# Performance work log

Measured on AMD Instinct MI355X. Metric: run time of the kernel, lower is better.

## Reference

```python
import jax, jax.numpy as jnp
import numpy as np

DIM = 512; H = 8; DH = 64; M = 256; ITERS = 6; K = 33  # residual conv kernel


def _pinv(x, iters=ITERS):
    # Moore-Penrose iterative pseudo-inverse (lucidrains moore_penrose_iter_pinv)
    abs_x = jnp.abs(x)
    denom = abs_x.sum(-1).max() * abs_x.sum(-2).max()  # global max of col/row sums
    z = jnp.swapaxes(x, -1, -2) / denom
    I = jnp.eye(x.shape[-1], dtype=x.dtype)
    for _ in range(iters):
        xz = x @ z
        z = 0.25 * z @ (13. * I - xz @ (15. * I - xz @ (7. * I - xz)))
    return z


def setup_inputs() -> dict:
    key = jax.random.key(0)
    ks = jax.random.split(key, 5)
    b, n = 4, 4096
    inner = H * DH
    x = jax.random.normal(ks[0], (b, n, DIM), jnp.float32)
    ln_g = jnp.ones((DIM,), jnp.float32)
    ln_b = jnp.zeros((DIM,), jnp.float32)
    w_qkv = jax.random.normal(ks[1], (DIM, 3 * inner), jnp.float32) / np.sqrt(DIM).astype(np.float32)
    w_out = jax.random.normal(ks[2], (inner, DIM), jnp.float32) / np.sqrt(inner).astype(np.float32)
    b_out = jnp.zeros((DIM,), jnp.float32)
    res_w = jax.random.normal(ks[3], (H, K), jnp.float32) * 0.02  # depthwise conv weight per head
    return {"x": x, "ln_g": ln_g, "ln_b": ln_b, "w_qkv": w_qkv,
            "w_out": w_out, "b_out": b_out, "res_w": res_w}


def reference(x, ln_g, ln_b, w_qkv, w_out, b_out, res_w):
    b, n, d = x.shape
    # LayerNorm (eps=1e-5, biased variance, like torch)
    mu = x.mean(-1, keepdims=True)
    var = ((x - mu) ** 2).mean(-1, keepdims=True)
    xn = (x - mu) * jax.lax.rsqrt(var + 1e-5) * ln_g + ln_b
    # QKV projection, no bias
    qkv = xn @ w_qkv  # [b, n, 3*h*dh]
    q, k, v = jnp.split(qkv, 3, axis=-1)
    tohd = lambda t: t.reshape(b, n, H, DH).transpose(0, 2, 1, 3)  # b h n d
    q = tohd(q) * (DH ** -0.5)
    k = tohd(k)
    v = tohd(v)
    # landmarks: mean over consecutive blocks of l = n // M (n divisible by M here)
    l = n // M
    q_l = q.reshape(b, H, M, l, DH).mean(3)  # b h m d
    k_l = k.reshape(b, H, M, l, DH).mean(3)
    attn1 = jax.nn.softmax(jnp.einsum('bhid,bhjd->bhij', q, k_l), axis=-1)   # b h n m
    attn2 = jax.nn.softmax(jnp.einsum('bhid,bhjd->bhij', q_l, k_l), axis=-1)  # b h m m
    attn3 = jax.nn.softmax(jnp.einsum('bhid,bhjd->bhij', q_l, k), axis=-1)   # b h m n
    out = (attn1 @ _pinv(attn2)) @ (attn3 @ v)  # b h n dh
    # depthwise residual conv over sequence dim (Conv2d(heads, heads, (33,1), groups=heads))
    res = jax.lax.conv_general_dilated(
        v, res_w.reshape(H, 1, K, 1), (1, 1), ((K // 2, K // 2), (0, 0)),
        feature_group_count=H, dimension_numbers=('NCHW', 'OIHW', 'NCHW'))
    out = out + res
    # merge heads + output projection (dropout is identity at eval)
    out = out.transpose(0, 2, 1, 3).reshape(b, n, H * DH) @ w_out + b_out
    # TransLayer residual
    return x + out
```

## Files before the change

kernel.cpp:

```cpp
#include <hip/hip_runtime.h>
#include <hip/hip_bf16.h>

#define SEQ    4096
#define NBAT   4
#define NHEAD  8
#define NBH    32
#define DMODEL 512
#define DHEAD  64
#define NLM    256
#define NSP    4

typedef __attribute__((ext_vector_type(8))) short s8v;
typedef __attribute__((ext_vector_type(4))) float f4v;

__device__ __forceinline__ float b2f(unsigned short u){
  union { unsigned int i; float f; } v; v.i = ((unsigned int)u) << 16; return v.f;
}
__device__ __forceinline__ unsigned short f2b(float f){
  union { float f; unsigned int i; } v; v.f = f;
  unsigned int r = v.i + 0x7fffu + ((v.i >> 16) & 1u);
  return (unsigned short)(r >> 16);
}
__device__ __forceinline__ s8v ldg8(const unsigned short* p){
  return *reinterpret_cast<const s8v*>(p);
}
__device__ __forceinline__ f4v mfma16(s8v a, s8v b, f4v c){
  return __builtin_amdgcn_mfma_f32_16x16x32_bf16(a, b, c, 0, 0, 0);
}
__device__ __forceinline__ f4v zero4(){ f4v z; z[0]=0.f; z[1]=0.f; z[2]=0.f; z[3]=0.f; return z; }
__device__ __forceinline__ void gload16(const unsigned short* g, unsigned short* l){
  __builtin_amdgcn_global_load_lds((const __attribute__((address_space(1))) unsigned int*)g,
                                   (__attribute__((address_space(3))) unsigned int*)l, 16, 0, 0);
}

__global__ void k_prep(const float* __restrict__ wqkv, const float* __restrict__ wout,
                       unsigned short* __restrict__ wqkvT, unsigned short* __restrict__ woutT,
                       unsigned int* __restrict__ denomU){
  int t = blockIdx.x*256 + threadIdx.x;
  if (t == 0) denomU[0] = 0u;
  if (t < 786432){ int kk = t/1536, n = t%1536; wqkvT[(size_t)n*512 + kk] = f2b(wqkv[t]); }
  else { int t2 = t - 786432; if (t2 < 262144){ int kk = t2/512, n = t2%512; woutT[(size_t)n*512 + kk] = f2b(wout[t2]); } }
}

__global__ __launch_bounds__(256) void k_ln(const float* __restrict__ x, const float* __restrict__ g,
                                            const float* __restrict__ be, unsigned short* __restrict__ xn){
  int row = blockIdx.x*4 + (threadIdx.x>>6);
  int l = threadIdx.x & 63;
  const float* xr = x + (size_t)row*DMODEL;
  float4 a = *(const float4*)(xr + l*4);
  float4 b = *(const float4*)(xr + 256 + l*4);
  float s = a.x+a.y+a.z+a.w + b.x+b.y+b.z+b.w;
  float q = a.x*a.x+a.y*a.y+a.z*a.z+a.w*a.w + b.x*b.x+b.y*b.y+b.z*b.z+b.w*b.w;
  #pragma unroll
  for (int m=1;m<64;m<<=1){ s += __shfl_xor(s,m); q += __shfl_xor(q,m); }
  float mean = s*(1.f/DMODEL);
  float rstd = rsqrtf(q*(1.f/DMODEL) - mean*mean + 1e-5f);
  int c0 = l*4, c1 = 256 + l*4;
  float av[4] = {a.x,a.y,a.z,a.w}, bv[4] = {b.x,b.y,b.z,b.w};
  ushort4 u0, u1;
  unsigned short* p0 = (unsigned short*)&u0; unsigned short* p1 = (unsigned short*)&u1;
  #pragma unroll
  for (int e=0;e<4;++e){
    p0[e] = f2b((av[e]-mean)*rstd*g[c0+e] + be[c0+e]);
    p1[e] = f2b((bv[e]-mean)*rstd*g[c1+e] + be[c1+e]);
  }
  *(ushort4*)(xn + (size_t)row*DMODEL + c0) = u0;
  *(ushort4*)(xn + (size_t)row*DMODEL + c1) = u1;
}

__device__ __forceinline__ void gemm512v2(const unsigned short* __restrict__ A, const unsigned short* __restrict__ B,
                                          int m0, int n0, int t, unsigned short* lA, unsigned short* lB,
                                          f4v acc[4][4]){
  int w = t>>6, l = t&63;
  int wm = (w&1)*64, wn = (w>>1)*64;
  int g = l>>4, qi = l&15;
  int rs = (w<<4) + (l>>2);
  int s0 = l&3;
  int c0 = ((s0 ^ ((rs>>1)&3)) << 3);
  int r1 = rs + 64;
  int c1 = ((s0 ^ ((r1>>1)&3)) << 3);
  const unsigned short* gA0 = A + (size_t)(m0+rs)*DMODEL + c0;
  const unsigned short* gA1 = A + (size_t)(m0+r1)*DMODEL + c1;
  const unsigned short* gB0 = B + (size_t)(n0+rs)*DMODEL + c0;
  const unsigned short* gB1 = B + (size_t)(n0+r1)*DMODEL + c1;
  unsigned short* dA0 = lA + (w<<9);
  unsigned short* dA1 = lA + 2048 + (w<<9);
  unsigned short* dB0 = lB + (w<<9);
  unsigned short* dB1 = lB + 2048 + (w<<9);
  int aofs[4], bofs[4];
  #pragma unroll
  for (int i=0;i<4;++i){
    int ra = wm + i*16 + qi;
    aofs[i] = ra*32 + ((g ^ ((ra>>1)&3))<<3);
    int rb = wn + i*16 + qi;
    bofs[i] = rb*32 + ((g ^ ((rb>>1)&3))<<3);
  }
  for (int ks=0; ks<16; ++ks){
    gload16(gA0, dA0); gload16(gA1, dA1);
    gload16(gB0, dB0); gload16(gB1, dB1);
    gA0 += 32; gA1 += 32; gB0 += 32; gB1 += 32;
    __syncthreads();
    s8v af[4], bf[4];
    #pragma unroll
    for (int i=0;i<4;++i) af[i] = *(s8v*)&lA[aofs[i]];
    #pragma unroll
    for (int j=0;j<4;++j) bf[j] = *(s8v*)&lB[bofs[j]];
    #pragma unroll
    for (int i=0;i<4;++i)
      #pragma unroll
      for (int j=0;j<4;++j) acc[i][j] = mfma16(af[i], bf[j], acc[i][j]);
    __syncthreads();
  }
}

__global__ __launch_bounds__(256) void k_gqkv(const unsigned short* __restrict__ xn, const unsigned short* __restrict__ wT,
                                              unsigned short* __restrict__ q, unsigned short* __restrict__ k,
                                              unsigned short* __restrict__ v, unsigned short* __restrict__ vT){
  __shared__ __align__(16) unsigned short lA[4096], lB[4096];
  int b0 = blockIdx.x;
  int bid = (b0 & 7) * 192 + (b0 >> 3);
  int mblk = bid/12, nblk = bid%12;
  int m0 = mblk*128, n0 = nblk*128;
  int t = threadIdx.x;
  f4v acc[4][4];
  #pragma unroll
  for (int i=0;i<4;++i)
    #pragma unroll
    for (int j=0;j<4;++j) acc[i][j] = zero4();
  gemm512v2(xn, wT, m0, n0, t, lA, lB, acc);
  int w = t>>6, l = t&63; int wm = (w&1)*64, wn = (w>>1)*64;
  int part = nblk >> 2;
  int coff = (nblk & 3) * 128;
  unsigned short* dst = (part==0) ? q : (part==1) ? k : v;
  float scale = (part==0) ? 0.125f : 1.f;
  #pragma unroll
  for (int i=0;i<4;++i)
  #pragma unroll
  for (int j=0;j<4;++j){
    int colg = coff + wn + j*16 + (l&15);
    int h = colg>>6, c = colg&63;
    #pragma unroll
    for (int r=0;r<4;++r){
      int rowg = m0 + wm + i*16 + ((l>>4)<<2) + r;
      int b = rowg>>12, n = rowg&4095;
      unsigned short val = f2b(acc[i][j][r]*scale);
      dst[ (((size_t)(b*NHEAD + h))*SEQ + n)*DHEAD + c ] = val;
      if (part == 2)
        vT[ (((size_t)(b*NHEAD + h))*DHEAD + c)*SEQ + n ] = val;
    }
  }
}

__global__ __launch_bounds__(256) void k_gout(const unsigned short* __restrict__ ao, const unsigned short* __restrict__ wT,
                                              const float* __restrict__ x, const float* __restrict__ bo,
                                              float* __restrict__ out){
  __shared__ __align__(16) unsigned short lA[4096], lB[4096];
  int b0 = blockIdx.x;
  int bid = (b0 & 7) * 64 + (b0 >> 3);
  int mblk = bid>>2, nblk = bid&3;
  int m0 = mblk*128, n0 = nblk*128;
  int t = threadIdx.x;
  f4v acc[4][4];
  #pragma unroll
  for (int i=0;i<4;++i)
    #pragma unroll
    for (int j=0;j<4;++j) acc[i][j] = zero4();
  gemm512v2(ao, wT, m0, n0, t, lA, lB, acc);
  int w = t>>6, l = t&63; int wm = (w&1)*64, wn = (w>>1)*64;
  #pragma unroll
  for (int i=0;i<4;++i)
  #pragma unroll
  for (int j=0;j<4;++j){
    int colg = n0 + wn + j*16 + (l&15);
    #pragma unroll
    for (int r=0;r<4;++r){
      int rowg = m0 + wm + i*16 + ((l>>4)<<2) + r;
      size_t ad = (size_t)rowg*DMODEL + colg;
      out[ad] = acc[i][j][r] + x[ad] + bo[colg];
    }
  }
}

__global__ void k_lmk(const unsigned short* __restrict__ q, const unsigned short* __restrict__ k,
                      unsigned short* __restrict__ ql, unsigned short* __restrict__ kl){
  int tg = blockIdx.x*256 + threadIdx.x;
  int c4 = (tg&15)*4, m = (tg>>4)&255, bh = tg>>12;
  const unsigned short* qb = q + ((size_t)bh*SEQ + m*16)*DHEAD + c4;
  const unsigned short* kb = k + ((size_t)bh*SEQ + m*16)*DHEAD + c4;
  float s0=0.f,s1=0.f,s2=0.f,s3=0.f, t0=0.f,t1=0.f,t2=0.f,t3=0.f;
  #pragma unroll
  for (int j=0;j<16;++j){
    ushort4 uq = *(const ushort4*)(qb + (size_t)j*DHEAD);
    ushort4 uk = *(const ushort4*)(kb + (size_t)j*DHEAD);
    s0+=b2f(uq.x); s1+=b2f(uq.y); s2+=b2f(uq.z); s3+=b2f(uq.w);
    t0+=b2f(uk.x); t1+=b2f(uk.y); t2+=b2f(uk.z); t3+=b2f(uk.w);
  }
  ushort4 oq, ok;
  oq.x=f2b(s0*(1.f/16.f)); oq.y=f2b(s1*(1.f/16.f)); oq.z=f2b(s2*(1.f/16.f)); oq.w=f2b(s3*(1.f/16.f));
  ok.x=f2b(t0*(1.f/16.f)); ok.y=f2b(t1*(1.f/16.f)); ok.z=f2b(t2*(1.f/16.f)); ok.w=f2b(t3*(1.f/16.f));
  *(ushort4*)(ql + ((size_t)bh*NLM + m)*DHEAD + c4) = oq;
  *(ushort4*)(kl + ((size_t)bh*NLM + m)*DHEAD + c4) = ok;
}

__global__ __launch_bounds__(512) void k_attn2(const unsigned short* __restrict__ ql, const unsigned short* __restrict__ kl,
                                               unsigned short* __restrict__ a2, unsigned short* __restrict__ a2t,
                                               unsigned int* __restrict__ denomU){
  __shared__ float cs[256];
  int bh = blockIdx.x; int t = threadIdx.x; int w = t>>6, l = t&63;
  const unsigned short* Q = ql + (size_t)bh*NLM*DHEAD;
  const unsigned short* K = kl + (size_t)bh*NLM*DHEAD;
  f4v acc[2][16];
  #pragma unroll
  for (int i=0;i<2;++i)
    #pragma unroll
    for (int j=0;j<16;++j) acc[i][j] = zero4();
  int m0 = w*32;
  #pragma unroll
  for (int ks=0; ks<2; ++ks){
    int kk = ks*32 + ((l>>4)<<3);
    s8v af0 = ldg8(&Q[(size_t)(m0 + (l&15))*DHEAD + kk]);
    s8v af1 = ldg8(&Q[(size_t)(m0 + 16 + (l&15))*DHEAD + kk]);
    #pragma unroll
    for (int j=0;j<16;++j){
      s8v bf = ldg8(&K[(size_t)(j*16 + (l&15))*DHEAD + kk]);
      acc[0][j] = mfma16(af0, bf, acc[0][j]);
      acc[1][j] = mfma16(af1, bf, acc[1][j]);
    }
  }
  #pragma unroll
  for (int i=0;i<2;++i)
  #pragma unroll
  for (int r=0;r<4;++r){
    float mx = -1e30f;
    #pragma unroll
    for (int j=0;j<16;++j) mx = fmaxf(mx, acc[i][j][r]);
    #pragma unroll
    for (int mm=1;mm<16;mm<<=1) mx = fmaxf(mx, __shfl_xor(mx,mm));
    float sm = 0.f;
    #pragma unroll
    for (int j=0;j<16;++j){ float p = __expf(acc[i][j][r]-mx); acc[i][j][r]=p; sm += p; }
    #pragma unroll
    for (int mm=1;mm<16;mm<<=1) sm += __shfl_xor(sm,mm);
    float inv = 1.f/sm;
    #pragma unroll
    for (int j=0;j<16;++j) acc[i][j][r] *= inv;
  }
  for (int e=t; e<256; e+=512) cs[e] = 0.f;
  __syncthreads();
  size_t b0 = (size_t)bh*NLM*NLM;
  #pragma unroll
  for (int i=0;i<2;++i)
  #pragma unroll
  for (int j=0;j<16;++j){
    int col = j*16 + (l&15);
    int rowb = m0 + i*16 + ((l>>4)<<2);
    float csp = 0.f;
    #pragma unroll
    for (int r=0;r<4;++r){
      float p = acc[i][j][r];
      unsigned short pb = f2b(p);
      a2 [b0 + (size_t)(rowb+r)*NLM + col] = pb;
      a2t[b0 + (size_t)col*NLM + rowb + r] = pb;
      csp += p;
    }
    csp += __shfl_xor(csp, 16); csp += __shfl_xor(csp, 32);
    if ((l>>4) == 0) atomicAdd(&cs[col], csp);
  }
  __syncthreads();
  if (t < 256) atomicMax(denomU, __float_as_uint(cs[t]));
}

__global__ __launch_bounds__(256) void k_a3w2p(const unsigned short* __restrict__ ql, const unsigned short* __restrict__ kb,
                                               const unsigned short* __restrict__ vT,
                                               float* __restrict__ po, float* __restrict__ pm, float* __restrict__ pd){
  __shared__ __align__(16) unsigned short Ks[256*64];
  __shared__ __align__(16) unsigned short Vs[64*256];
  int bid = blockIdx.x;
  int ksp = bid & 3;
  int qp  = (bid >> 2) & 3;
  int bh  = bid >> 4;
  int t = threadIdx.x, w = t>>6, l = t&63;
  int q0 = qp*64 + w*16;
  int g = l>>4, qi = l&15;
  const unsigned short* Q = ql + ((size_t)bh*NLM + q0)*DHEAD;
  const unsigned short* K = kb + (size_t)bh*SEQ*DHEAD;
  const unsigned short* V = vT + (size_t)bh*DHEAD*SEQ;
  s8v bq0 = ldg8(&Q[(size_t)qi*DHEAD + g*8]);
  s8v bq1 = ldg8(&Q[(size_t)qi*DHEAD + 32 + g*8]);
  float m_run = -1e30f, den = 0.f;
  f4v oacc[4];
  #pragma unroll
  for (int j=0;j<4;++j) oacc[j] = zero4();
  int sl0 = ((g&1)*2)*16 + qi;
  int jsel = g>>1;
  for (int kc = ksp*4; kc < ksp*4+4; ++kc){
    const unsigned short* Kc = K + (size_t)kc*256*DHEAD;
    #pragma unroll
    for (int it2=0; it2<8; ++it2){
      int cid = it2*256 + t;
      int row = cid>>3, cl = cid&7;
      gload16(&Kc[(size_t)(row<<6) + ((cl^(row&7))<<3)], Ks + it2*2048 + w*512);
      int row2 = cid>>5, cl2 = cid&31;
      gload16(&V[(size_t)row2*SEQ + kc*256 + ((cl2^(row2&7))<<3)], Vs + it2*2048 + 16384 - 16384 + w*512 + 0);
    }
    __syncthreads();
    f4v acc[16];
    #pragma unroll
    for (int j=0;j<16;++j) acc[j] = zero4();
    #pragma unroll
    for (int ks=0;ks<2;++ks){
      s8v bq = (ks==0) ? bq0 : bq1;
      #pragma unroll
      for (int j=0;j<16;++j){
        int r = j*16+qi;
        s8v ak = *(s8v*)&Ks[(size_t)(r<<6) + (((ks*4+g) ^ (qi&7))<<3)];
        acc[j] = mfma16(ak, bq, acc[j]);
      }
    }
    float cm = -1e30f;
    #pragma unroll
    for (int j=0;j<16;++j)
      cm = fmaxf(cm, fmaxf(fmaxf(acc[j][0],acc[j][1]), fmaxf(acc[j][2],acc[j][3])));
    cm = fmaxf(cm, __shfl_xor(cm,16));
    cm = fmaxf(cm, __shfl_xor(cm,32));
    float nm = fmaxf(m_run, cm);
    float f = __expf(m_run - nm);
    m_run = nm;
    float ls = 0.f;
    unsigned int pku[32];
    #pragma unroll
    for (int j=0;j<16;++j){
      float p0 = __expf(acc[j][0]-nm), p1 = __expf(acc[j][1]-nm);
      float p2 = __expf(acc[j][2]-nm), p3 = __expf(acc[j][3]-nm);
      ls += (p0+p1)+(p2+p3);
      pku[2*j+0] = (unsigned int)f2b(p0) | ((unsigned int)f2b(p1)<<16);
      pku[2*j+1] = (unsigned int)f2b(p2) | ((unsigned int)f2b(p3)<<16);
    }
    den = den*f + ls;
    float fr0 = __shfl(f, g*4+0, 64), fr1 = __shfl(f, g*4+1, 64);
    float fr2 = __shfl(f, g*4+2, 64), fr3 = __shfl(f, g*4+3, 64);
    #pragma unroll
    for (int j=0;j<4;++j){
      oacc[j][0]*=fr0; oacc[j][1]*=fr1; oacc[j][2]*=fr2; oacc[j][3]*=fr3;
    }
    #pragma unroll
    for (int ks=0;ks<8;++ks){
      unsigned int w0a = (unsigned int)__shfl((int)pku[4*ks+0], sl0, 64);
      unsigned int w1a = (unsigned int)__shfl((int)pku[4*ks+1], sl0, 64);
      unsigned int w0b = (unsigned int)__shfl((int)pku[4*ks+2], sl0, 64);
      unsigned int w1b = (unsigned int)__shfl((int)pku[4*ks+3], sl0, 64);
      unsigned int w2a = (unsigned int)__shfl((int)pku[4*ks+0], sl0+16, 64);
      unsigned int w3a = (unsigned int)__shfl((int)pku[4*ks+1], sl0+16, 64);
      unsigned int w2b = (unsigned int)__shfl((int)pku[4*ks+2], sl0+16, 64);
      unsigned int w3b = (unsigned int)__shfl((int)pku[4*ks+3], sl0+16, 64);
      unsigned int wv0 = jsel ? w0b : w0a;
      unsigned int wv1 = jsel ? w1b : w1a;
      unsigned int wv2 = jsel ? w2b : w2a;
      unsigned int wv3 = jsel ? w3b : w3a;
      s8v af;
      af[0] = (short)(wv0&0xffff); af[1] = (short)(wv0>>16);
      af[2] = (short)(wv1&0xffff); af[3] = (short)(wv1>>16);
      af[4] = (short)(wv2&0xffff); af[5] = (short)(wv2>>16);
      af[6] = (short)(wv3&0xffff); af[7] = (short)(wv3>>16);
      int ch = ks*4 + g;
      #pragma unroll
      for (int j=0;j<4;++j){
        int r = j*16+qi;
        s8v bu = *(s8v*)&Vs[(size_t)(r<<8) + ((ch ^ (qi&7))<<3)];
        oacc[j] = mfma16(af, bu, oacc[j]);
      }
    }
    __syncthreads();
  }
  den += __shfl_xor(den,16); den += __shfl_xor(den,32);
  #pragma unroll
  for (int j=0;j<4;++j)
    #pragma unroll
    for (int r=0;r<4;++r)
      po[(((size_t)(ksp*NBH + bh))*NLM + q0 + g*4 + r)*DHEAD + j*16 + qi] = oacc[j][r];
  if (g == 0){
    pm[(size_t)(ksp*NBH + bh)*NLM + q0 + qi] = m_run;
    pd[(size_t)(ksp*NBH + bh)*NLM + q0 + qi] = den;
  }
}

__global__ __launch_bounds__(256) void k_a3c(const float* __restrict__ po, const float* __restrict__ pm,
                                             const float* __restrict__ pd, unsigned short* __restrict__ w2t){
  int tg = blockIdx.x*256 + threadIdx.x;
  int bh = tg >> 12; int c = (tg >> 6) & 63; int r4 = (tg & 63) << 2;
  ushort4 ov;
  unsigned short* op = (unsigned short*)&ov;
  #pragma unroll
  for (int rr=0; rr<4; ++rr){
    int row = r4 + rr;
    float m[NSP];
    float gm = -1e30f;
    #pragma unroll
    for (int s=0;s<NSP;++s){ m[s] = pm[(size_t)(s*NBH+bh)*NLM + row]; gm = fmaxf(gm, m[s]); }
    float den = 0.f, o = 0.f;
    #pragma unroll
    for (int s=0;s<NSP;++s){
      float wsc = __expf(m[s]-gm);
      den += pd[(size_t)(s*NBH+bh)*NLM + row]*wsc;
      o   += po[(((size_t)(s*NBH+bh))*NLM + row)*DHEAD + c]*wsc;
    }
    op[rr] = f2b(o/den);
  }
  *(ushort4*)&w2t[(size_t)bh*DHEAD*NLM + (size_t)c*NLM + r4] = ov;
}

__global__ __launch_bounds__(256) void k_conv(const unsigned short* __restrict__ v, const float* __restrict__ rw,
                                              unsigned short* __restrict__ cf){
  int bh = blockIdx.x >> 6;
  int n0 = (blockIdx.x & 63) * 64;
  int h = bh & 7, b = bh >> 3;
  int t = threadIdx.x;
  int tx = t & 15, ty = t >> 4;
  int c4 = tx * 4;
  int nb = n0 + ty * 4;
  const unsigned short* vb = v + ((size_t)bh * SEQ) * DHEAD + c4;
  ushort4 val[36];
  #pragma unroll
  for (int i = 0; i < 36; ++i){
    int nn = nb - 16 + i;
    if (nn >= 0 && nn < SEQ) val[i] = *(const ushort4*)(vb + (size_t)nn * DHEAD);
    else { val[i].x = 0; val[i].y = 0; val[i].z = 0; val[i].w = 0; }
  }
  float wgt[33];
  #pragma unroll
  for (int o = 0; o < 33; ++o) wgt[o] = rw[h*33 + o];
  #pragma unroll
  for (int i = 0; i < 4; ++i){
    float s0 = 0.f, s1 = 0.f, s2 = 0.f, s3 = 0.f;
    #pragma unroll
    for (int o = 0; o < 33; ++o){
      ushort4 u = val[i + o];
      float w0 = wgt[o];
      s0 += w0 * b2f(u.x); s1 += w0 * b2f(u.y);
      s2 += w0 * b2f(u.z); s3 += w0 * b2f(u.w);
    }
    ushort4 ov;
    ov.x = f2b(s0); ov.y = f2b(s1); ov.z = f2b(s2); ov.w = f2b(s3);
    size_t ad = ((size_t)b * SEQ + (nb + i)) * DMODEL + h * DHEAD + c4;
    *(ushort4*)(cf + ad) = ov;
  }
}

__device__ __forceinline__ void pcore(const unsigned short* __restrict__ Ab, const unsigned short* __restrict__ Bb,
                                      int m0, int n0, int l, f4v acc[4][4]){
  for (int ks=0; ks<8; ++ks){
    int kk = ks*32 + ((l>>4)<<3);
    s8v af[4], bf[4];
    #pragma unroll
    for (int i=0;i<4;++i) af[i] = ldg8(&Ab[(size_t)(m0 + i*16 + (l&15))*256 + kk]);
    #pragma unroll
    for (int j=0;j<4;++j) bf[j] = ldg8(&Bb[(size_t)(n0 + j*16 + (l&15))*256 + kk]);
    #pragma unroll
    for (int i=0;i<4;++i)
      #pragma unroll
      for (int j=0;j<4;++j) acc[i][j] = mfma16(af[i], bf[j], acc[i][j]);
  }
}


__global__ __launch_bounds__(64) void k_x0(const unsigned short* __restrict__ a2,
                                           unsigned short* __restrict__ XN, unsigned short* __restrict__ XT,
                                           const unsigned int* __restrict__ denomU){
  int bid = blockIdx.x;
  int bh = bid>>4, tt = bid&15;
  int m0 = (tt>>2)*64, n0 = (tt&3)*64;
  int l = threadIdx.x;
  size_t bb = (size_t)bh*65536;
  f4v acc[4][4];
  #pragma unroll
  for (int i=0;i<4;++i)
    #pragma unroll
    for (int j=0;j<4;++j) acc[i][j] = zero4();
  pcore(a2+bb, a2+bb, m0, n0, l, acc);
  float s = 1.f/__uint_as_float(denomU[0]);
  #pragma unroll
  for (int i=0;i<4;++i)
  #pragma unroll
  for (int j=0;j<4;++j){
    int col = n0 + j*16 + (l&15);
    #pragma unroll
    for (int r=0;r<4;++r){
      int row = m0 + i*16 + ((l>>4)<<2) + r;
      unsigned short ob = f2b(acc[i][j][r]*s);
      XN[bb + (size_t)row*256 + col] = ob;
      XT[bb + (size_t)col*256 + row] = ob;
    }
  }
}

__global__ __launch_bounds__(64) void k_l1(const unsigned short* __restrict__ XN, const unsigned short* __restrict__ XT,
                                           const unsigned short* __restrict__ zsrc,
                                           unsigned short* __restrict__ YN, unsigned short* __restrict__ YT,
                                           unsigned short* __restrict__ CT,
                                           unsigned short* __restrict__ WN, unsigned short* __restrict__ EN){
  int bid = blockIdx.x;
  int part = bid>>9; bid &= 511;
  int bh = bid>>4, tt = bid&15;
  int m0 = (tt>>2)*64, n0 = (tt&3)*64;
  int l = threadIdx.x;
  size_t bb = (size_t)bh*65536;
  f4v acc[4][4];
  #pragma unroll
  for (int i=0;i<4;++i)
    #pragma unroll
    for (int j=0;j<4;++j) acc[i][j] = zero4();
  if (part == 0){
    pcore(XN+bb, XT+bb, m0, n0, l, acc);
    #pragma unroll
    for (int i=0;i<4;++i)
    #pragma unroll
    for (int j=0;j<4;++j){
      int col = n0 + j*16 + (l&15);
      #pragma unroll
      for (int r=0;r<4;++r){
        int row = m0 + i*16 + ((l>>4)<<2) + r;
        float y = acc[i][j][r];
        float xv = b2f(XN[bb + (size_t)row*256 + col]);
        unsigned short yb = f2b(y);
        YN[bb + (size_t)row*256 + col] = yb;
        YT[bb + (size_t)col*256 + row] = yb;
        CT[bb + (size_t)col*256 + row] = f2b(7.f*xv - y);
      }
    }
  } else {
    pcore(zsrc+bb, XT+bb, m0, n0, l, acc);
    #pragma unroll
    for (int i=0;i<4;++i)
    #pragma unroll
    for (int j=0;j<4;++j){
      int col = n0 + j*16 + (l&15);
      #pragma unroll
      for (int r=0;r<4;++r){
        int row = m0 + i*16 + ((l>>4)<<2) + r;
        size_t idx = bb + (size_t)row*256 + col;
        float wv = acc[i][j][r];
        float zv = b2f(zsrc[idx]);
        WN[idx] = f2b(wv);
        EN[idx] = f2b(7.f*zv - wv);
      }
    }
  }
}

__global__ __launch_bounds__(64) void k_l2(unsigned short* __restrict__ XN, unsigned short* __restrict__ XT,
                                           const unsigned short* __restrict__ zsrc, unsigned short* __restrict__ zdst,
                                           const unsigned short* __restrict__ YN, const unsigned short* __restrict__ YT,
                                           const unsigned short* __restrict__ CT,
                                           const unsigned short* __restrict__ WN, const unsigned short* __restrict__ EN,
                                           int zonly){
  int bid = blockIdx.x;
  int part;
  if (zonly){ part = 1; } else { part = bid>>9; bid &= 511; }
  int bh = bid>>4, tt = bid&15;
  int m0 = (tt>>2)*64, n0 = (tt&3)*64;
  int l = threadIdx.x;
  size_t bb = (size_t)bh*65536;
  f4v acc[4][4];
  #pragma unroll
  for (int i=0;i<4;++i)
    #pragma unroll
    for (int j=0;j<4;++j) acc[i][j] = zero4();
  if (part == 0){
    pcore(YN+bb, CT+bb, m0, n0, l, acc);
    #pragma unroll
    for (int i=0;i<4;++i)
    #pragma unroll
    for (int j=0;j<4;++j){
      int col = n0 + j*16 + (l&15);
      #pragma unroll
      for (int r=0;r<4;++r){
        int row = m0 + i*16 + ((l>>4)<<2) + r;
        size_t idx = bb + (size_t)row*256 + col;
        float xv = b2f(XN[idx]);
        float yv = b2f(YN[idx]);
        unsigned short ob = f2b(0.25f*(13.f*xv - 15.f*yv + acc[i][j][r]));
        XN[idx] = ob;
        XT[bb + (size_t)col*256 + row] = ob;
      }
    }
  } else {
    pcore(EN+bb, YT+bb, m0, n0, l, acc);
    #pragma unroll
    for (int i=0;i<4;++i)
    #pragma unroll
    for (int j=0;j<4;++j){
      int col = n0 + j*16 + (l&15);
      #pragma unroll
      for (int r=0;r<4;++r){
        int row = m0 + i*16 + ((l>>4)<<2) + r;
        size_t idx = bb + (size_t)row*256 + col;
        float zv = b2f(zsrc[idx]);
        float wv = b2f(WN[idx]);
        zdst[idx] = f2b(0.25f*(13.f*zv - 15.f*wv + acc[i][j][r]));
      }
    }
  }
}

__global__ __launch_bounds__(64) void k_ue(const unsigned short* __restrict__ z6, const unsigned short* __restrict__ w2t,
                                           unsigned short* __restrict__ ut, const unsigned int* __restrict__ denomU){
  int bid = blockIdx.x;
  int bh = bid>>2, tt = bid&3;
  int m0 = tt*64;
  int l = threadIdx.x;
  float dinv = 1.f/__uint_as_float(denomU[0]);
  f4v acc[4][4];
  #pragma unroll
  for (int i=0;i<4;++i)
    #pragma unroll
    for (int j=0;j<4;++j) acc[i][j] = zero4();
  pcore(z6 + (size_t)bh*65536, w2t + (size_t)bh*16384, m0, 0, l, acc);
  #pragma unroll
  for (int i=0;i<4;++i)
  #pragma unroll
  for (int j=0;j<4;++j){
    int col = j*16 + (l&15);
    #pragma unroll
    for (int r=0;r<4;++r){
      int row = m0 + i*16 + ((l>>4)<<2) + r;
      ut[(size_t)bh*16384 + (size_t)col*256 + row] = f2b(acc[i][j][r]*dinv);
    }
  }
}

__global__ __launch_bounds__(256) void k_attn1(const unsigned short* __restrict__ qb, const unsigned short* __restrict__ kl,
                                               const unsigned short* __restrict__ ut, const unsigned short* __restrict__ cf,
                                               unsigned short* __restrict__ ao){
  int bh = blockIdx.x>>6;
  int t = threadIdx.x, w = t>>6, l = t&63;
  int q0 = ((blockIdx.x&63)<<6) + (w<<4);
  int g = l>>4, qi = l&15;
  const unsigned short* Q = qb + (size_t)bh*SEQ*DHEAD;
  const unsigned short* K = kl + (size_t)bh*NLM*DHEAD;
  f4v acc[16];
  #pragma unroll
  for (int j=0;j<16;++j) acc[j] = zero4();
  #pragma unroll
  for (int ks=0;ks<2;++ks){
    int kk = ks*32 + g*8;
    s8v bq = ldg8(&Q[(size_t)(q0+qi)*DHEAD + kk]);
    #pragma unroll
    for (int j=0;j<16;++j){
      s8v ak = ldg8(&K[(size_t)(j*16+qi)*DHEAD + kk]);
      acc[j] = mfma16(ak, bq, acc[j]);
    }
  }
  float mx = -1e30f;
  #pragma unroll
  for (int j=0;j<16;++j)
    mx = fmaxf(mx, fmaxf(fmaxf(acc[j][0],acc[j][1]), fmaxf(acc[j][2],acc[j][3])));
  mx = fmaxf(mx, __shfl_xor(mx,16));
  mx = fmaxf(mx, __shfl_xor(mx,32));
  float sm = 0.f;
  #pragma unroll
  for (int j=0;j<16;++j)
    #pragma unroll
    for (int r=0;r<4;++r){ float p = __expf(acc[j][r]-mx); acc[j][r]=p; sm += p; }
  sm += __shfl_xor(sm,16); sm += __shfl_xor(sm,32);
  float inv = 1.f/sm;
  unsigned int pku[32];
  #pragma unroll
  for (int j=0;j<16;++j){
    pku[2*j+0] = (unsigned int)f2b(acc[j][0]*inv) | ((unsigned int)f2b(acc[j][1]*inv)<<16);
    pku[2*j+1] = (unsigned int)f2b(acc[j][2]*inv) | ((unsigned int)f2b(acc[j][3]*inv)<<16);
  }
  const unsigned short* U = ut + (size_t)bh*DHEAD*NLM;
  f4v oacc[4];
  #pragma unroll
  for (int j=0;j<4;++j) oacc[j] = zero4();
  int sl0 = ((g&1)*2)*16 + qi;
  int jsel = g>>1;
  #pragma unroll
  for (int ks=0;ks<8;++ks){
    unsigned int w0a = (unsigned int)__shfl((int)pku[4*ks+0], sl0, 64);
    unsigned int w1a = (unsigned int)__shfl((int)pku[4*ks+1], sl0, 64);
    unsigned int w0b = (unsigned int)__shfl((int)pku[4*ks+2], sl0, 64);
    unsigned int w1b = (unsigned int)__shfl((int)pku[4*ks+3], sl0, 64);
    unsigned int w2a = (unsigned int)__shfl((int)pku[4*ks+0], sl0+16, 64);
    unsigned int w3a = (unsigned int)__shfl((int)pku[4*ks+1], sl0+16, 64);
    unsigned int w2b = (unsigned int)__shfl((int)pku[4*ks+2], sl0+16, 64);
    unsigned int w3b = (unsigned int)__shfl((int)pku[4*ks+3], sl0+16, 64);
    unsigned int wv0 = jsel ? w0b : w0a;
    unsigned int wv1 = jsel ? w1b : w1a;
    unsigned int wv2 = jsel ? w2b : w2a;
    unsigned int wv3 = jsel ? w3b : w3a;
    s8v af;
    af[0] = (short)(wv0&0xffff); af[1] = (short)(wv0>>16);
    af[2] = (short)(wv1&0xffff); af[3] = (short)(wv1>>16);
    af[4] = (short)(wv2&0xffff); af[5] = (short)(wv2>>16);
    af[6] = (short)(wv3&0xffff); af[7] = (short)(wv3>>16);
    int mk = ks*32 + g*8;
    #pragma unroll
    for (int j=0;j<4;++j){
      s8v bu = ldg8(&U[(size_t)(j*16+qi)*NLM + mk]);
      oacc[j] = mfma16(af, bu, oacc[j]);
    }
  }
  int b = bh>>3, h = bh&7;
  #pragma unroll
  for (int j=0;j<4;++j){
    int c = j*16 + qi;
    #pragma unroll
    for (int r=0;r<4;++r){
      int n = q0 + g*4 + r;
      size_t ad = ((size_t)(b*SEQ + n))*DMODEL + h*DHEAD + c;
      ao[ad] = f2b(oacc[j][r] + b2f(cf[ad]));
    }
  }
}

extern "C" void kernel_launch(void* const* d_in, const int* in_sizes, int n_in,
                              void* d_out, int out_size, void* d_ws, size_t ws_size,
                              hipStream_t stream){
  const float* x    = (const float*)d_in[0];
  const float* lng  = (const float*)d_in[1];
  const float* lnb  = (const float*)d_in[2];
  const float* wqkv = (const float*)d_in[3];
  const float* wout = (const float*)d_in[4];
  const float* bout = (const float*)d_in[5];
  const float* resw = (const float*)d_in[6];
  float* out = (float*)d_out;

  char* ws = (char*)d_ws;
  size_t off = 0;
  auto alloc = [&](size_t bytes)->char*{ char* p = ws + off; off += (bytes + 255) & ~(size_t)255; return p; };

  unsigned short* wqkvT = (unsigned short*)alloc((size_t)1536*512*2);
  unsigned short* woutT = (unsigned short*)alloc((size_t)512*512*2);
  unsigned int*   denomU= (unsigned int*)  alloc(256);
  unsigned short* xn    = (unsigned short*)alloc((size_t)16384*512*2);
  unsigned short* XN = xn;
  unsigned short* XT = xn + (size_t)1*NBH*NLM*NLM;
  unsigned short* YN = xn + (size_t)2*NBH*NLM*NLM;
  unsigned short* YT = xn + (size_t)3*NBH*NLM*NLM;
  unsigned short* q   = (unsigned short*)alloc((size_t)NBH*SEQ*DHEAD*2);
  unsigned short* kb  = (unsigned short*)alloc((size_t)NBH*SEQ*DHEAD*2);
  unsigned short* ao  = kb;
  unsigned short* v   = (unsigned short*)alloc((size_t)NBH*SEQ*DHEAD*2);
  unsigned short* vT  = (unsigned short*)alloc((size_t)NBH*DHEAD*SEQ*2);
  unsigned short* ql  = (unsigned short*)alloc((size_t)NBH*NLM*DHEAD*2);
  unsigned short* kl  = (unsigned short*)alloc((size_t)NBH*NLM*DHEAD*2);
  unsigned short* a2  = (unsigned short*)alloc((size_t)NBH*NLM*NLM*2);
  unsigned short* a2t = (unsigned short*)alloc((size_t)NBH*NLM*NLM*2);
  unsigned short* convf = (unsigned short*)alloc((size_t)NBAT*SEQ*DMODEL*2);
  unsigned short* CTb = (unsigned short*)alloc((size_t)NBH*NLM*NLM*2);
  unsigned short* WN  = (unsigned short*)alloc((size_t)NBH*NLM*NLM*2);
  unsigned short* EN  = (unsigned short*)alloc((size_t)NBH*NLM*NLM*2);
  unsigned short* zP  = (unsigned short*)alloc((size_t)NBH*NLM*NLM*2);
  unsigned short* zQ  = (unsigned short*)alloc((size_t)NBH*NLM*NLM*2);
  float* po = (float*)alloc((size_t)NSP*NBH*NLM*DHEAD*4);
  float* pm = (float*)alloc((size_t)NSP*NBH*NLM*4);
  float* pd = (float*)alloc((size_t)NSP*NBH*NLM*4);
  unsigned short* w2t = (unsigned short*)alloc((size_t)NBH*DHEAD*NLM*2);
  unsigned short* ut  = (unsigned short*)alloc((size_t)NBH*DHEAD*NLM*2);
  (void)ws_size; (void)in_sizes; (void)n_in; (void)out_size;

  k_prep<<<4096,256,0,stream>>>(wqkv, wout, wqkvT, woutT, denomU);
  k_ln  <<<4096,256,0,stream>>>(x, lng, lnb, xn);
  k_gqkv<<<1536,256,0,stream>>>(xn, wqkvT, q, kb, v, vT);
  k_lmk <<<512,256,0,stream>>>(q, kb, ql, kl);
  k_attn2<<<32,512,0,stream>>>(ql, kl, a2, a2t, denomU);
  k_a3w2p<<<512,256,0,stream>>>(ql, kb, vT, po, pm, pd);
  k_a3c <<<512,256,0,stream>>>(po, pm, pd, w2t);
  k_conv<<<2048,256,0,stream>>>(v, resw, convf);

  k_x0<<<512,64,0,stream>>>(a2, XN, XT, denomU);
  unsigned short* zbuf[2] = {zP, zQ};
  const unsigned short* zs = a2t;
  for (int it = 0; it < 6; ++it){
    int zonly = (it==5) ? 1 : 0;
    k_l1<<<1024,64,0,stream>>>(XN, XT, zs, YN, YT, CTb, WN, EN);
    k_l2<<<zonly?512:1024,64,0,stream>>>(XN, XT, zs, zbuf[it&1], YN, YT, CTb, WN, EN, zonly);
    zs = zbuf[it&1];
  }
  k_ue<<<128,64,0,stream>>>(zs, w2t, ut, denomU);

  k_attn1<<<2048,256,0,stream>>>(q, kl, ut, convf, ao);
  k_gout <<<512,256,0,stream>>>(ao, woutT, x, bout, out);
}
```

Before: 566.5 us.

## Merge prep/LN and conv/landmark kernels; drop transposed copies in pinv iterations

Fuses the weight-conversion and LayerNorm kernels into one launch, and likewise the depthwise conv and landmark-mean kernels, to cut launch overhead and let independent work share the GPU. The pinv iteration no longer writes transposed copies (XT, YT, CT) and instead passes the same row-major buffer as the B operand to pcore, relying on symmetry or on pcore's operand convention to remove scattered transposed stores. The transposed-store removal is only correct if the matrices involved are symmetric or pcore reads B in the matching orientation, so it carries a correctness risk.

Measured after the change: 516.4 us. 1.1x faster.

```diff
diff --git a/kernel.cpp b/kernel.cpp
--- a/kernel.cpp
+++ b/kernel.cpp
@@ -33,39 +33,41 @@
                                    (__attribute__((address_space(3))) unsigned int*)l, 16, 0, 0);
 }
 
-__global__ void k_prep(const float* __restrict__ wqkv, const float* __restrict__ wout,
-                       unsigned short* __restrict__ wqkvT, unsigned short* __restrict__ woutT,
-                       unsigned int* __restrict__ denomU){
-  int t = blockIdx.x*256 + threadIdx.x;
-  if (t == 0) denomU[0] = 0u;
-  if (t < 786432){ int kk = t/1536, n = t%1536; wqkvT[(size_t)n*512 + kk] = f2b(wqkv[t]); }
-  else { int t2 = t - 786432; if (t2 < 262144){ int kk = t2/512, n = t2%512; woutT[(size_t)n*512 + kk] = f2b(wout[t2]); } }
-}
-
-__global__ __launch_bounds__(256) void k_ln(const float* __restrict__ x, const float* __restrict__ g,
-                                            const float* __restrict__ be, unsigned short* __restrict__ xn){
-  int row = blockIdx.x*4 + (threadIdx.x>>6);
-  int l = threadIdx.x & 63;
-  const float* xr = x + (size_t)row*DMODEL;
-  float4 a = *(const float4*)(xr + l*4);
-  float4 b = *(const float4*)(xr + 256 + l*4);
-  float s = a.x+a.y+a.z+a.w + b.x+b.y+b.z+b.w;
-  float q = a.x*a.x+a.y*a.y+a.z*a.z+a.w*a.w + b.x*b.x+b.y*b.y+b.z*b.z+b.w*b.w;
-  #pragma unroll
-  for (int m=1;m<64;m<<=1){ s += __shfl_xor(s,m); q += __shfl_xor(q,m); }
-  float mean = s*(1.f/DMODEL);
-  float rstd = rsqrtf(q*(1.f/DMODEL) - mean*mean + 1e-5f);
-  int c0 = l*4, c1 = 256 + l*4;
-  float av[4] = {a.x,a.y,a.z,a.w}, bv[4] = {b.x,b.y,b.z,b.w};
-  ushort4 u0, u1;
-  unsigned short* p0 = (unsigned short*)&u0; unsigned short* p1 = (unsigned short*)&u1;
-  #pragma unroll
-  for (int e=0;e<4;++e){
-    p0[e] = f2b((av[e]-mean)*rstd*g[c0+e] + be[c0+e]);
-    p1[e] = f2b((bv[e]-mean)*rstd*g[c1+e] + be[c1+e]);
-  }
-  *(ushort4*)(xn + (size_t)row*DMODEL + c0) = u0;
-  *(ushort4*)(xn + (size_t)row*DMODEL + c1) = u1;
+__global__ __launch_bounds__(256) void k_prepln(const float* __restrict__ wqkv, const float* __restrict__ wout,
+                                                const float* __restrict__ x, const float* __restrict__ g,
+                                                const float* __restrict__ be,
+                                                unsigned short* __restrict__ wqkvT, unsigned short* __restrict__ woutT,
+                                                unsigned short* __restrict__ xn, unsigned int* __restrict__ denomU){
+  int b0 = blockIdx.x;
+  if (b0 < 4096){
+    int t = b0*256 + threadIdx.x;
+    if (t == 0) denomU[0] = 0u;
+    if (t < 786432){ int kk = t/1536, n = t%1536; wqkvT[(size_t)n*512 + kk] = f2b(wqkv[t]); }
+    else { int t2 = t - 786432; if (t2 < 262144){ int kk = t2/512, n = t2%512; woutT[(size_t)n*512 + kk] = f2b(wout[t2]); } }
+  } else {
+    int row = (b0 - 4096)*4 + (threadIdx.x>>6);
+    int l = threadIdx.x & 63;
+    const float* xr = x + (size_t)row*DMODEL;
+    float4 a = *(const float4*)(xr + l*4);
+    float4 b = *(const float4*)(xr + 256 + l*4);
+    float s = a.x+a.y+a.z+a.w + b.x+b.y+b.z+b.w;
+    float q = a.x*a.x+a.y*a.y+a.z*a.z+a.w*a.w + b.x*b.x+b.y*b.y+b.z*b.z+b.w*b.w;
+    #pragma unroll
+    for (int m=1;m<64;m<<=1){ s += __shfl_xor(s,m); q += __shfl_xor(q,m); }
+    float mean = s*(1.f/DMODEL);
+    float rstd = rsqrtf(q*(1.f/DMODEL) - mean*mean + 1e-5f);
+    int c0 = l*4, c1 = 256 + l*4;
+    float av[4] = {a.x,a.y,a.z,a.w}, bv[4] = {b.x,b.y,b.z,b.w};
+    ushort4 u0, u1;
+    unsigned short* p0 = (unsigned short*)&u0; unsigned short* p1 = (unsigned short*)&u1;
+    #pragma unroll
+    for (int e=0;e<4;++e){
+      p0[e] = f2b((av[e]-mean)*rstd*g[c0+e] + be[c0+e]);
+      p1[e] = f2b((bv[e]-mean)*rstd*g[c1+e] + be[c1+e]);
+    }
+    *(ushort4*)(xn + (size_t)row*DMODEL + c0) = u0;
+    *(ushort4*)(xn + (size_t)row*DMODEL + c1) = u1;
+  }
 }
 
 __device__ __forceinline__ void gemm512v2(const unsigned short* __restrict__ A, const unsigned short* __restrict__ B,
@@ -181,25 +183,64 @@
   }
 }
 
-__global__ void k_lmk(const unsigned short* __restrict__ q, const unsigned short* __restrict__ k,
-                      unsigned short* __restrict__ ql, unsigned short* __restrict__ kl){
-  int tg = blockIdx.x*256 + threadIdx.x;
-  int c4 = (tg&15)*4, m = (tg>>4)&255, bh = tg>>12;
-  const unsigned short* qb = q + ((size_t)bh*SEQ + m*16)*DHEAD + c4;
-  const unsigned short* kb = k + ((size_t)bh*SEQ + m*16)*DHEAD + c4;
-  float s0=0.f,s1=0.f,s2=0.f,s3=0.f, t0=0.f,t1=0.f,t2=0.f,t3=0.f;
-  #pragma unroll
-  for (int j=0;j<16;++j){
-    ushort4 uq = *(const ushort4*)(qb + (size_t)j*DHEAD);
-    ushort4 uk = *(const ushort4*)(kb + (size_t)j*DHEAD);
-    s0+=b2f(uq.x); s1+=b2f(uq.y); s2+=b2f(uq.z); s3+=b2f(uq.w);
-    t0+=b2f(uk.x); t1+=b2f(uk.y); t2+=b2f(uk.z); t3+=b2f(uk.w);
-  }
-  ushort4 oq, ok;
-  oq.x=f2b(s0*(1.f/16.f)); oq.y=f2b(s1*(1.f/16.f)); oq.z=f2b(s2*(1.f/16.f)); oq.w=f2b(s3*(1.f/16.f));
-  ok.x=f2b(t0*(1.f/16.f)); ok.y=f2b(t1*(1.f/16.f)); ok.z=f2b(t2*(1.f/16.f)); ok.w=f2b(t3*(1.f/16.f));
-  *(ushort4*)(ql + ((size_t)bh*NLM + m)*DHEAD + c4) = oq;
-  *(ushort4*)(kl + ((size_t)bh*NLM + m)*DHEAD + c4) = ok;
+__global__ __launch_bounds__(256) void k_cvlmk(const unsigned short* __restrict__ q, const unsigned short* __restrict__ k,
+                                               const unsigned short* __restrict__ v, const float* __restrict__ rw,
+                                               unsigned short* __restrict__ cf,
+                                               unsigned short* __restrict__ ql, unsigned short* __restrict__ kl){
+  int blk = blockIdx.x;
+  if (blk < 2048){
+    int bh = blk >> 6;
+    int n0 = (blk & 63) * 64;
+    int h = bh & 7, b = bh >> 3;
+    int t = threadIdx.x;
+    int tx = t & 15, ty = t >> 4;
+    int c4 = tx * 4;
+    int nb = n0 + ty * 4;
+    const unsigned short* vb = v + ((size_t)bh * SEQ) * DHEAD + c4;
+    ushort4 val[36];
+    #pragma unroll
+    for (int i = 0; i < 36; ++i){
+      int nn = nb - 16 + i;
+      if (nn >= 0 && nn < SEQ) val[i] = *(const ushort4*)(vb + (size_t)nn * DHEAD);
+      else { val[i].x = 0; val[i].y = 0; val[i].z = 0; val[i].w = 0; }
+    }
+    float wgt[33];
+    #pragma unroll
+    for (int o = 0; o < 33; ++o) wgt[o] = rw[h*33 + o];
+    #pragma unroll
+    for (int i = 0; i < 4; ++i){
+      float s0 = 0.f, s1 = 0.f, s2 = 0.f, s3 = 0.f;
+      #pragma unroll
+      for (int o = 0; o < 33; ++o){
+        ushort4 u = val[i + o];
+        float w0 = wgt[o];
+        s0 += w0 * b2f(u.x); s1 += w0 * b2f(u.y);
+        s2 += w0 * b2f(u.z); s3 += w0 * b2f(u.w);
+      }
+      ushort4 ov;
+      ov.x = f2b(s0); ov.y = f2b(s1); ov.z = f2b(s2); ov.w = f2b(s3);
+      size_t ad = ((size_t)b * SEQ + (nb + i)) * DMODEL + h * DHEAD + c4;
+      *(ushort4*)(cf + ad) = ov;
+    }
+  } else {
+    int tg = (blk - 2048)*256 + threadIdx.x;
+    int c4 = (tg&15)*4, m = (tg>>4)&255, bh = tg>>12;
+    const unsigned short* qb = q + ((size_t)bh*SEQ + m*16)*DHEAD + c4;
+    const unsigned short* kb = k + ((size_t)bh*SEQ + m*16)*DHEAD + c4;
+    float s0=0.f,s1=0.f,s2=0.f,s3=0.f, t0=0.f,t1=0.f,t2=0.f,t3=0.f;
+    #pragma unroll
+    for (int j=0;j<16;++j){
+      ushort4 uq = *(const ushort4*)(qb + (size_t)j*DHEAD);
+      ushort4 uk = *(const ushort4*)(kb + (size_t)j*DHEAD);
+      s0+=b2f(uq.x); s1+=b2f(uq.y); s2+=b2f(uq.z); s3+=b2f(uq.w);
+      t0+=b2f(uk.x); t1+=b2f(uk.y); t2+=b2f(uk.z); t3+=b2f(uk.w);
+    }
+    ushort4 oq, ok;
+    oq.x=f2b(s0*(1.f/16.f)); oq.y=f2b(s1*(1.f/16.f)); oq.z=f2b(s2*(1.f/16.f)); oq.w=f2b(s3*(1.f/16.f));
+    ok.x=f2b(t0*(1.f/16.f)); ok.y=f2b(t1*(1.f/16.f)); ok.z=f2b(t2*(1.f/16.f)); ok.w=f2b(t3*(1.f/16.f));
+    *(ushort4*)(ql + ((size_t)bh*NLM + m)*DHEAD + c4) = oq;
+    *(ushort4*)(kl + ((size_t)bh*NLM + m)*DHEAD + c4) = ok;
+  }
 }
 
 __global__ __launch_bounds__(512) void k_attn2(const unsigned short* __restrict__ ql, const unsigned short* __restrict__ kl,
@@ -301,7 +342,7 @@
       int row = cid>>3, cl = cid&7;
       gload16(&Kc[(size_t)(row<<6) + ((cl^(row&7))<<3)], Ks + it2*2048 + w*512);
       int row2 = cid>>5, cl2 = cid&31;
-      gload16(&V[(size_t)row2*SEQ + kc*256 + ((cl2^(row2&7))<<3)], Vs + it2*2048 + 16384 - 16384 + w*512 + 0);
+      gload16(&V[(size_t)row2*SEQ + kc*256 + ((cl2^(row2&7))<<3)], Vs + it2*2048 + w*512);
     }
     __syncthreads();
     f4v acc[16];
@@ -409,43 +450,6 @@
   *(ushort4*)&w2t[(size_t)bh*DHEAD*NLM + (size_t)c*NLM + r4] = ov;
 }
 
-__global__ __launch_bounds__(256) void k_conv(const unsigned short* __restrict__ v, const float* __restrict__ rw,
-                                              unsigned short* __restrict__ cf){
-  int bh = blockIdx.x >> 6;
-  int n0 = (blockIdx.x & 63) * 64;
-  int h = bh & 7, b = bh >> 3;
-  int t = threadIdx.x;
-  int tx = t & 15, ty = t >> 4;
-  int c4 = tx * 4;
-  int nb = n0 + ty * 4;
-  const unsigned short* vb = v + ((size_t)bh * SEQ) * DHEAD + c4;
-  ushort4 val[36];
-  #pragma unroll
-  for (int i = 0; i < 36; ++i){
-    int nn = nb - 16 + i;
-    if (nn >= 0 && nn < SEQ) val[i] = *(const ushort4*)(vb + (size_t)nn * DHEAD);
-    else { val[i].x = 0; val[i].y = 0; val[i].z = 0; val[i].w = 0; }
-  }
-  float wgt[33];
-  #pragma unroll
-  for (int o = 0; o < 33; ++o) wgt[o] = rw[h*33 + o];
-  #pragma unroll
-  for (int i = 0; i < 4; ++i){
-    float s0 = 0.f, s1 = 0.f, s2 = 0.f, s3 = 0.f;
-    #pragma unroll
-    for (int o = 0; o < 33; ++o){
-      ushort4 u = val[i + o];
-      float w0 = wgt[o];
-      s0 += w0 * b2f(u.x); s1 += w0 * b2f(u.y);
-      s2 += w0 * b2f(u.z); s3 += w0 * b2f(u.w);
-    }
-    ushort4 ov;
-    ov.x = f2b(s0); ov.y = f2b(s1); ov.z = f2b(s2); ov.w = f2b(s3);
-    size_t ad = ((size_t)b * SEQ + (nb + i)) * DMODEL + h * DHEAD + c4;
-    *(ushort4*)(cf + ad) = ov;
-  }
-}
-
 __device__ __forceinline__ void pcore(const unsigned short* __restrict__ Ab, const unsigned short* __restrict__ Bb,
                                       int m0, int n0, int l, f4v acc[4][4]){
   for (int ks=0; ks<8; ++ks){
@@ -464,7 +468,7 @@
 
 
 __global__ __launch_bounds__(64) void k_x0(const unsigned short* __restrict__ a2,
-                                           unsigned short* __restrict__ XN, unsigned short* __restrict__ XT,
+                                           unsigned short* __restrict__ XS,
                                            const unsigned int* __restrict__ denomU){
   int bid = blockIdx.x;
   int bh = bid>>4, tt = bid&15;
@@ -486,17 +490,14 @@
     #pragma unroll
     for (int r=0;r<4;++r){
       int row = m0 + i*16 + ((l>>4)<<2) + r;
-      unsigned short ob = f2b(acc[i][j][r]*s);
-      XN[bb + (size_t)row*256 + col] = ob;
-      XT[bb + (size_t)col*256 + row] = ob;
-    }
-  }
-}
-
-__global__ __launch_bounds__(64) void k_l1(const unsigned short* __restrict__ XN, const unsigned short* __restrict__ XT,
+      XS[bb + (size_t)row*256 + col] = f2b(acc[i][j][r]*s);
+    }
+  }
+}
+
+__global__ __launch_bounds__(64) void k_l1(const unsigned short* __restrict__ XS,
                                            const unsigned short* __restrict__ zsrc,
-                                           unsigned short* __restrict__ YN, unsigned short* __restrict__ YT,
-                                           unsigned short* __restrict__ CT,
+                                           unsigned short* __restrict__ YS, unsigned short* __restrict__ CS,
                                            unsigned short* __restrict__ WN, unsigned short* __restrict__ EN){
   int bid = blockIdx.x;
   int part = bid>>9; bid &= 511;
@@ -510,7 +511,7 @@
     #pragma unroll
     for (int j=0;j<4;++j) acc[i][j] = zero4();
   if (part == 0){
-    pcore(XN+bb, XT+bb, m0, n0, l, acc);
+    pcore(XS+bb, XS+bb, m0, n0, l, acc);
     #pragma unroll
     for (int i=0;i<4;++i)
     #pragma unroll
@@ -519,16 +520,15 @@
       #pragma unroll
       for (int r=0;r<4;++r){
         int row = m0 + i*16 + ((l>>4)<<2) + r;
+        size_t idx = bb + (size_t)row*256 + col;
         float y = acc[i][j][r];
-        float xv = b2f(XN[bb + (size_t)row*256 + col]);
-        unsigned short yb = f2b(y);
-        YN[bb + (size_t)row*256 + col] = yb;
-        YT[bb + (size_t)col*256 + row] = yb;
-        CT[bb + (size_t)col*256 + row] = f2b(7.f*xv - y);
+        float xv = b2f(XS[idx]);
+        YS[idx] = f2b(y);
+        CS[idx] = f2b(7.f*xv - y);
       }
     }
   } else {
-    pcore(zsrc+bb, XT+bb, m0, n0, l, acc);
+    pcore(zsrc+bb, XS+bb, m0, n0, l, acc);
     #pragma unroll
     for (int i=0;i<4;++i)
     #pragma unroll
@@ -547,10 +547,9 @@
   }
 }
 
-__global__ __launch_bounds__(64) void k_l2(unsigned short* __restrict__ XN, unsigned short* __restrict__ XT,
+__global__ __launch_bounds__(64) void k_l2(unsigned short* __restrict__ XS,
                                            const unsigned short* __restrict__ zsrc, unsigned short* __restrict__ zdst,
-                                           const unsigned short* __restrict__ YN, const unsigned short* __restrict__ YT,
-                                           const unsigned short* __restrict__ CT,
+                                           const unsigned short* __restrict__ YS, const unsigned short* __restrict__ CS,
                                            const unsigned short* __restrict__ WN, const unsigned short* __restrict__ EN,
                                            int zonly){
   int bid = blockIdx.x;
@@ -566,7 +565,7 @@
     #pragma unroll
     for (int j=0;j<4;++j) acc[i][j] = zero4();
   if (part == 0){
-    pcore(YN+bb, CT+bb, m0, n0, l, acc);
+    pcore(YS+bb, CS+bb, m0, n0, l, acc);
     #pragma unroll
     for (int i=0;i<4;++i)
     #pragma unroll
@@ -576,15 +575,13 @@
       for (int r=0;r<4;++r){
         int row = m0 + i*16 + ((l>>4)<<2) + r;
         size_t idx = bb + (size_t)row*256 + col;
-        float xv = b2f(XN[idx]);
-        float yv = b2f(YN[idx]);
-        unsigned short ob = f2b(0.25f*(13.f*xv - 15.f*yv + acc[i][j][r]));
-        XN[idx] = ob;
-        XT[bb + (size_t)col*256 + row] = ob;
+        float xv = b2f(XS[idx]);
+        float yv = b2f(YS[idx]);
+        XS[idx] = f2b(0.25f*(13.f*xv - 15.f*yv + acc[i][j][r]));
       }
     }
   } else {
-    pcore(EN+bb, YT+bb, m0, n0, l, acc);
+    pcore(EN+bb, YS+bb, m0, n0, l, acc);
     #pragma unroll
     for (int i=0;i<4;++i)
     #pragma unroll
@@ -734,10 +731,9 @@
   unsigned short* woutT = (unsigned short*)alloc((size_t)512*512*2);
   unsigned int*   denomU= (unsigned int*)  alloc(256);
   unsigned short* xn    = (unsigned short*)alloc((size_t)16384*512*2);
-  unsigned short* XN = xn;
-  unsigned short* XT = xn + (size_t)1*NBH*NLM*NLM;
-  unsigned short* YN = xn + (size_t)2*NBH*NLM*NLM;
-  unsigned short* YT = xn + (size_t)3*NBH*NLM*NLM;
+  unsigned short* XS = xn;
+  unsigned short* YS = xn + (size_t)1*NBH*NLM*NLM;
+  unsigned short* CS = xn + (size_t)2*NBH*NLM*NLM;
   unsigned short* q   = (unsigned short*)alloc((size_t)NBH*SEQ*DHEAD*2);
   unsigned short* kb  = (unsigned short*)alloc((size_t)NBH*SEQ*DHEAD*2);
   unsigned short* ao  = kb;
@@ -748,7 +744,6 @@
   unsigned short* a2  = (unsigned short*)alloc((size_t)NBH*NLM*NLM*2);
   unsigned short* a2t = (unsigned short*)alloc((size_t)NBH*NLM*NLM*2);
   unsigned short* convf = (unsigned short*)alloc((size_t)NBAT*SEQ*DMODEL*2);
-  unsigned short* CTb = (unsigned short*)alloc((size_t)NBH*NLM*NLM*2);
   unsigned short* WN  = (unsigned short*)alloc((size_t)NBH*NLM*NLM*2);
   unsigned short* EN  = (unsigned short*)alloc((size_t)NBH*NLM*NLM*2);
   unsigned short* zP  = (unsigned short*)alloc((size_t)NBH*NLM*NLM*2);
@@ -760,22 +755,20 @@
   unsigned short* ut  = (unsigned short*)alloc((size_t)NBH*DHEAD*NLM*2);
   (void)ws_size; (void)in_sizes; (void)n_in; (void)out_size;
 
-  k_prep<<<4096,256,0,stream>>>(wqkv, wout, wqkvT, woutT, denomU);
-  k_ln  <<<4096,256,0,stream>>>(x, lng, lnb, xn);
+  k_prepln<<<8192,256,0,stream>>>(wqkv, wout, x, lng, lnb, wqkvT, woutT, xn, denomU);
   k_gqkv<<<1536,256,0,stream>>>(xn, wqkvT, q, kb, v, vT);
-  k_lmk <<<512,256,0,stream>>>(q, kb, ql, kl);
+  k_cvlmk<<<2560,256,0,stream>>>(q, kb, v, resw, convf, ql, kl);
   k_attn2<<<32,512,0,stream>>>(ql, kl, a2, a2t, denomU);
   k_a3w2p<<<512,256,0,stream>>>(ql, kb, vT, po, pm, pd);
   k_a3c <<<512,256,0,stream>>>(po, pm, pd, w2t);
-  k_conv<<<2048,256,0,stream>>>(v, resw, convf);
-
-  k_x0<<<512,64,0,stream>>>(a2, XN, XT, denomU);
+
+  k_x0<<<512,64,0,stream>>>(a2, XS, denomU);
   unsigned short* zbuf[2] = {zP, zQ};
   const unsigned short* zs = a2t;
   for (int it = 0; it < 6; ++it){
     int zonly = (it==5) ? 1 : 0;
-    k_l1<<<1024,64,0,stream>>>(XN, XT, zs, YN, YT, CTb, WN, EN);
-    k_l2<<<zonly?512:1024,64,0,stream>>>(XN, XT, zs, zbuf[it&1], YN, YT, CTb, WN, EN, zonly);
+    k_l1<<<1024,64,0,stream>>>(XS, zs, YS, CS, WN, EN);
+    k_l2<<<zonly?512:1024,64,0,stream>>>(XS, zs, zbuf[it&1], YS, CS, WN, EN, zonly);
     zs = zbuf[it&1];
   }
   k_ue<<<128,64,0,stream>>>(zs, w2t, ut, denomU);
```
